# Performance work log

Measured on AMD Instinct MI355X. Metric: run time of the kernel, lower is better.

The kernel has to match this reference:

```python
import jax, jax.numpy as jnp
import numpy as np
from jax.scipy.linalg import solve_triangular, cho_solve

K_SPARSE = 5
COMMIT = 0.25
EPS = 1e-10


def batch_omp(X, D, K):
    """Batched Orthogonal Matching Pursuit.
    X: [C, M] signals (columns). D: [C, N] L2-normalized dictionary.
    Returns support [M, K] (int32) and coefficients [M, K] in selection order.
    """
    G = D.T @ D                    # [N, N] Gram matrix
    h_bar = (D.T @ X).T            # [M, N] correlations
    M, N = h_bar.shape
    h = h_bar
    mask = jnp.ones((M, N), dtype=bool)
    gamma = jnp.zeros_like(h_bar)
    L = jnp.ones((M, 1, 1), dtype=X.dtype)
    rows = jnp.arange(M)
    I = None
    for k in range(1, K + 1):  # K is small and static -> unrolled
        idx = jnp.argmax(jnp.abs(h) * mask, axis=1)          # [M]
        mask = mask.at[rows, idx].set(False)
        if k > 1:
            G_col = G[I, idx[:, None]]                        # [M, k-1]
            w = solve_triangular(L, G_col[..., None], lower=True)[..., 0]  # [M, k-1]
            corner = jnp.sqrt(jnp.clip(1.0 - jnp.sum(w * w, axis=1), 1e-12))  # [M]
            top = jnp.concatenate([L, jnp.zeros((M, k - 1, 1), X.dtype)], axis=2)
            bot = jnp.concatenate([w[:, None, :], corner[:, None, None]], axis=2)
            L = jnp.concatenate([top, bot], axis=1)           # [M, k, k]
            I = jnp.concatenate([I, idx[:, None]], axis=1)
        else:
            I = idx[:, None]
        h_sel = h_bar[rows[:, None], I]                       # [M, k]
        gamma_sel = cho_solve((L, True), h_sel[..., None])[..., 0]  # [M, k]
        gamma = gamma.at[rows[:, None], I].set(gamma_sel)
        # beta = gamma_sel @ G[I]  -> residual update over all atoms
        beta = jnp.einsum('mk,mkn->mn', gamma_sel, G[I])      # [M, N]
        h = h_bar - beta
    coeffs = gamma[rows[:, None], I]                          # [M, K]
    return I, coeffs


def setup_inputs() -> dict:
    key = jax.random.key(0)
    k1, k2 = jax.random.split(key)
    z_e = jax.random.normal(k1, (8, 64, 64, 64), dtype=jnp.float32)        # [B, C, H, W]
    dictionary = jax.random.normal(k2, (64, 512), dtype=jnp.float32)       # [C, N]
    return {"z_e": z_e, "dictionary": dictionary}


def reference(z_e, dictionary):
    B, C, H, W = z_e.shape
    # [B,C,H,W] -> [C, B*H*W] column signals
    signals = z_e.transpose(0, 2, 3, 1).reshape(-1, C).T
    # L2-normalize dictionary columns (F.normalize with dim=0)
    norms = jnp.linalg.norm(dictionary, axis=0, keepdims=True)
    Dn = dictionary / jnp.maximum(norms, EPS)
    # OMP runs under no_grad in the original
    support, coeffs = batch_omp(jax.lax.stop_gradient(signals),
                                jax.lax.stop_gradient(Dn), K_SPARSE)
    # reconstruct: sum_k coeff_k * atom_k (gradient flows through Dn)
    atoms = Dn.T[support]                                     # [M, K, C]
    recon = jnp.einsum('mkc,mk->mc', atoms, coeffs)           # [M, C]
    z_dl = recon.reshape(B, H, W, C).transpose(0, 3, 1, 2)    # [B, C, H, W]
    dl_latent_loss = jnp.mean((z_dl - jax.lax.stop_gradient(z_e)) ** 2)
    e_latent_loss = jnp.mean((jax.lax.stop_gradient(z_dl) - z_e) ** 2)
    loss = dl_latent_loss + COMMIT * e_latent_loss
    z_dl_ste = z_e + jax.lax.stop_gradient(z_dl - z_e)        # straight-through
    return (z_dl_ste, loss,
            support.reshape(B, H, W, K_SPARSE),
            coeffs.reshape(B, H, W, K_SPARSE))
```

## Files before the change

### kernel.cpp

```cpp
#include <hip/hip_runtime.h>

#define NC 64
#define NA 512
#define KS 5

#define WS_DN   0
#define WS_DNT  32768
#define WS_G    65536
#define WS_ACCF 327680

#define OUT_LOSS 2097152
#define OUT_SUP  2097153
#define OUT_COF  2260993

__global__ void norm_kernel(const float* __restrict__ D, float* __restrict__ Dn,
                            float* __restrict__ DnT) {
  int n = blockIdx.x * 64 + threadIdx.x;
  float s = 0.f;
  for (int c = 0; c < NC; ++c) {
    float v = D[c * NA + n];
    s += v * v;
  }
  float den = fmaxf(sqrtf(s), 1e-10f);
  for (int c = 0; c < NC; ++c) {
    float v = D[c * NA + n] / den;
    Dn[c * NA + n]  = v;
    DnT[n * NC + c] = v;
  }
}

__global__ void gram_kernel(const float* __restrict__ Dn,
                            float* __restrict__ G, double* __restrict__ accum) {
  __shared__ float col[NC];
  int i = blockIdx.x, t = threadIdx.x;
  if (t < NC) col[t] = Dn[t * NA + i];
  if (i == 0 && t == 0) *accum = 0.0;
  __syncthreads();
  float s = 0.f;
#pragma unroll
  for (int c = 0; c < NC; ++c) s += col[c] * Dn[c * NA + t];
  G[(size_t)i * NA + t] = s;
}

template<int KK>
__device__ __forceinline__ void omp_stepH(
    const int hl, const float* __restrict__ G,
    const float* __restrict__ parkS,
    float (&h16)[16], unsigned &msk, int (&I)[KS],
    float (&Lo)[10], float (&rd)[KS], float (&gam)[KS]) {
  float bv = -1.f; int bn = 0;
#pragma unroll
  for (int s = 0; s < 16; ++s) {
    int a = ((s >> 2) << 7) + 4 * hl + (s & 3);
    float v = ((msk >> s) & 1u) ? fabsf(h16[s]) : 0.f;
    if (v > bv) { bv = v; bn = a; }
  }
#pragma unroll
  for (int off = 1; off < 32; off <<= 1) {
    float ov = __shfl_xor(bv, off);
    int   on = __shfl_xor(bn, off);
    if (ov > bv || (ov == bv && on < bn)) { bv = ov; bn = on; }
  }
  const int idx = bn;
  if (((idx & 127) >> 2) == hl)
    msk &= ~(1u << (((idx >> 7) << 2) | (idx & 3)));
  I[KK] = idx;

  if constexpr (KK < 4) {
    const float4* pk4 = (const float4*)parkS;
#pragma unroll
    for (int i = 0; i < 4; ++i) {
      float4 hv = pk4[(i << 5) + hl];
      h16[i*4+0] = hv.x; h16[i*4+1] = hv.y; h16[i*4+2] = hv.z; h16[i*4+3] = hv.w;
    }
  }

  if constexpr (KK == 0) {
    rd[0] = 1.f;
  } else {
    float Gc[KK], w_[KK];
#pragma unroll
    for (int j = 0; j < KK; ++j) Gc[j] = G[(size_t)I[j] * NA + idx];
#pragma unroll
    for (int i = 0; i < KK; ++i) {
      float ssum = Gc[i];
#pragma unroll
      for (int j = 0; j < i; ++j) ssum -= Lo[i*(i-1)/2 + j] * w_[j];
      w_[i] = ssum * rd[i];
    }
    float ww = 0.f;
#pragma unroll
    for (int i = 0; i < KK; ++i) ww += w_[i] * w_[i];
    float corner = sqrtf(fmaxf(1.f - ww, 1e-12f));
#pragma unroll
    for (int j = 0; j < KK; ++j) Lo[KK*(KK-1)/2 + j] = w_[j];
    rd[KK] = 1.f / corner;
  }

#pragma unroll
  for (int i = 0; i <= KK; ++i) {
    float b_ = parkS[I[i]];
#pragma unroll
    for (int j = 0; j < i; ++j) b_ -= Lo[i*(i-1)/2 + j] * gam[j];
    gam[i] = b_ * rd[i];
  }
#pragma unroll
  for (int i = KK; i >= 0; --i) {
    float g_ = gam[i];
#pragma unroll
    for (int j = i + 1; j <= KK; ++j) g_ -= Lo[j*(j-1)/2 + i] * gam[j];
    gam[i] = g_ * rd[i];
  }

  if constexpr (KK < 4) {
#pragma unroll
    for (int j = 0; j <= KK; ++j) {
      const float4* g4 = (const float4*)(G + (size_t)I[j] * NA);
      const float gj = gam[j];
#pragma unroll
      for (int i = 0; i < 4; ++i) {
        float4 g = g4[(i << 5) + hl];
        h16[i*4+0] -= gj * g.x; h16[i*4+1] -= gj * g.y;
        h16[i*4+2] -= gj * g.z; h16[i*4+3] -= gj * g.w;
      }
    }
  }
}

__global__ __launch_bounds__(256, 2) void omp_kernel(
    const float* __restrict__ z, const float* __restrict__ Dn,
    const float* __restrict__ DnT, const float* __restrict__ G,
    float* __restrict__ out, double* __restrict__ accum) {
  __shared__ __align__(16) float park[8 * NA];
  __shared__ float xsz[8 * NC];
  __shared__ double wsq[8];
  const int t = threadIdx.x, lane = t & 63, wv = t >> 6;
  const int hl = lane & 31;
  const int m0 = blockIdx.x * 8;
  const int bh = m0 >> 6, b = bh >> 6, h = bh & 63, w0 = m0 & 63;
  const size_t zbase = (size_t)b * 262144 + (size_t)h * 64 + w0;

  for (int j = t; j < 8 * NC; j += 256) {
    int c = j >> 3, s = j & 7;
    xsz[s * NC + c] = z[zbase + (size_t)c * 4096 + s];
  }
  __syncthreads();
  const int sig = wv * 2 + (lane >> 5);
  const float2 xf2 = *(const float2*)&xsz[sig * NC + 2 * hl];

  {
    float acc[8][2];
#pragma unroll
    for (int s = 0; s < 8; ++s) { acc[s][0] = 0.f; acc[s][1] = 0.f; }

    const float2* Dn2 = (const float2*)Dn + (wv << 6) + lane;
    const float4* zp4 = (const float4*)(z + zbase);
#pragma unroll 8
    for (int c = 0; c < 64; ++c) {
      float2 dv = Dn2[c << 8];
      float4 xa = zp4[(c << 10)];
      float4 xb = zp4[(c << 10) + 1];
      acc[0][0] += xa.x * dv.x; acc[0][1] += xa.x * dv.y;
      acc[1][0] += xa.y * dv.x; acc[1][1] += xa.y * dv.y;
      acc[2][0] += xa.z * dv.x; acc[2][1] += xa.z * dv.y;
      acc[3][0] += xa.w * dv.x; acc[3][1] += xa.w * dv.y;
      acc[4][0] += xb.x * dv.x; acc[4][1] += xb.x * dv.y;
      acc[5][0] += xb.y * dv.x; acc[5][1] += xb.y * dv.y;
      acc[6][0] += xb.z * dv.x; acc[6][1] += xb.z * dv.y;
      acc[7][0] += xb.w * dv.x; acc[7][1] += xb.w * dv.y;
    }
    float2* park2 = (float2*)park;
#pragma unroll
    for (int s = 0; s < 8; ++s)
      park2[(s << 8) + (wv << 6) + lane] = make_float2(acc[s][0], acc[s][1]);
  }
  __syncthreads();

  const float* parkS = park + (size_t)sig * NA;
  float h16[16];
  {
    const float4* pk4 = (const float4*)parkS;
#pragma unroll
    for (int i = 0; i < 4; ++i) {
      float4 hv = pk4[(i << 5) + hl];
      h16[i*4+0] = hv.x; h16[i*4+1] = hv.y; h16[i*4+2] = hv.z; h16[i*4+3] = hv.w;
    }
  }
  unsigned msk = 0xFFFFu;
  int I[KS];
  float Lo[10], rd[KS], gam[KS];

  omp_stepH<0>(hl, G, parkS, h16, msk, I, Lo, rd, gam);
  omp_stepH<1>(hl, G, parkS, h16, msk, I, Lo, rd, gam);
  omp_stepH<2>(hl, G, parkS, h16, msk, I, Lo, rd, gam);
  omp_stepH<3>(hl, G, parkS, h16, msk, I, Lo, rd, gam);
  omp_stepH<4>(hl, G, parkS, h16, msk, I, Lo, rd, gam);

  float rrA = 0.f, rrB = 0.f;
#pragma unroll
  for (int j = 0; j < KS; ++j) {
    const float2 dvv = ((const float2*)(DnT + (size_t)I[j] * NC))[hl];
    rrA += gam[j] * dvv.x;
    rrB += gam[j] * dvv.y;
  }
  const float dA = rrA - xf2.x, dB = rrB - xf2.y;
  xsz[(2 * hl) * 8 + sig]     = xf2.x + dA;
  xsz[(2 * hl + 1) * 8 + sig] = xf2.y + dB;
  double sq = (double)dA * (double)dA + (double)dB * (double)dB;
#pragma unroll
  for (int off = 1; off < 32; off <<= 1) sq += __shfl_xor(sq, off);
  if (hl == 0) wsq[sig] = sq;

  if (hl < KS) {
    int   iv = I[0];
    float gv = gam[0];
    if (hl == 1) { iv = I[1]; gv = gam[1]; }
    if (hl == 2) { iv = I[2]; gv = gam[2]; }
    if (hl == 3) { iv = I[3]; gv = gam[3]; }
    if (hl == 4) { iv = I[4]; gv = gam[4]; }
    const int m = m0 + sig;
    out[OUT_SUP + (size_t)m * KS + hl] = (float)iv;
    out[OUT_COF + (size_t)m * KS + hl] = gv;
  }

  __syncthreads();
  for (int j = t; j < 8 * NC; j += 256) {
    int c = j >> 3, s = j & 7;
    out[zbase + (size_t)c * 4096 + s] = xsz[j];
  }
  if (t == 0) {
    double ssum = 0.0;
#pragma unroll
    for (int i = 0; i < 8; ++i) ssum += wsq[i];
    atomicAdd(accum, ssum);
  }
}

__global__ void final_kernel(const double* __restrict__ accum, float* __restrict__ out) {
  double mse = *accum / 2097152.0;
  out[OUT_LOSS] = (float)(mse + 0.25 * mse);
}

extern "C" void kernel_launch(void* const* d_in, const int* in_sizes, int n_in,
                              void* d_out, int out_size, void* d_ws, size_t ws_size,
                              hipStream_t stream) {
  const float* z_e = (const float*)d_in[0];
  const float* dic = (const float*)d_in[1];
  float* out = (float*)d_out;
  float* ws = (float*)d_ws;
  float* Dn   = ws + WS_DN;
  float* DnT  = ws + WS_DNT;
  float* G    = ws + WS_G;
  double* accu = (double*)(ws + WS_ACCF);

  hipLaunchKernelGGL(norm_kernel,  dim3(8),    dim3(64),  0, stream, dic, Dn, DnT);
  hipLaunchKernelGGL(gram_kernel,  dim3(NA),   dim3(NA),  0, stream, Dn, G, accu);
  hipLaunchKernelGGL(omp_kernel,   dim3(4096), dim3(256), 0, stream,
                     z_e, Dn, DnT, G, out, accu);
  hipLaunchKernelGGL(final_kernel, dim3(1),    dim3(1),   0, stream, accu, out);
}
```

Baseline: 152.3 us.

## Alias xsz into park LDS, fuse final loss kernel, simplify argmax

Several changes land together. The separate xsz and wsq shared buffers now alias the park buffer, which cuts LDS per block and may allow more resident blocks, at the cost of an extra barrier. The final loss kernel is folded into the OMP kernel through a last-block ticket counter, which removes one launch. The argmax becomes a two-pass max followed by a min-index reduction, and the selected h_bar value is cached in registers. Together these aim to cut launch overhead, LDS pressure and shuffle count.

```diff
diff --git a/kernel.cpp b/kernel.cpp
--- a/kernel.cpp
+++ b/kernel.cpp
@@ -30,11 +30,12 @@
 }
 
 __global__ void gram_kernel(const float* __restrict__ Dn,
-                            float* __restrict__ G, double* __restrict__ accum) {
+                            float* __restrict__ G, double* __restrict__ accum,
+                            unsigned* __restrict__ ticket) {
   __shared__ float col[NC];
   int i = blockIdx.x, t = threadIdx.x;
   if (t < NC) col[t] = Dn[t * NA + i];
-  if (i == 0 && t == 0) *accum = 0.0;
+  if (i == 0 && t == 0) { *accum = 0.0; *ticket = 0u; }
   __syncthreads();
   float s = 0.f;
 #pragma unroll
@@ -47,24 +48,32 @@
     const int hl, const float* __restrict__ G,
     const float* __restrict__ parkS,
     float (&h16)[16], unsigned &msk, int (&I)[KS],
-    float (&Lo)[10], float (&rd)[KS], float (&gam)[KS]) {
-  float bv = -1.f; int bn = 0;
-#pragma unroll
-  for (int s = 0; s < 16; ++s) {
+    float (&Lo)[10], float (&rd)[KS], float (&gam)[KS], float (&hbI)[KS]) {
+#define MVAL(s) ((((msk) >> (s)) & 1u) ? fabsf(h16[s]) : 0.f)
+  float m0 = fmaxf(MVAL(0), MVAL(1)),   m1 = fmaxf(MVAL(2), MVAL(3));
+  float m2 = fmaxf(MVAL(4), MVAL(5)),   m3 = fmaxf(MVAL(6), MVAL(7));
+  float m4 = fmaxf(MVAL(8), MVAL(9)),   m5 = fmaxf(MVAL(10), MVAL(11));
+  float m6 = fmaxf(MVAL(12), MVAL(13)), m7 = fmaxf(MVAL(14), MVAL(15));
+  float bv = fmaxf(fmaxf(fmaxf(m0, m1), fmaxf(m2, m3)),
+                   fmaxf(fmaxf(m4, m5), fmaxf(m6, m7)));
+#pragma unroll
+  for (int off = 1; off < 32; off <<= 1)
+    bv = fmaxf(bv, __shfl_xor(bv, off));
+  int cand = 0x7FFFFFFF;
+#pragma unroll
+  for (int s = 15; s >= 0; --s) {
     int a = ((s >> 2) << 7) + 4 * hl + (s & 3);
-    float v = ((msk >> s) & 1u) ? fabsf(h16[s]) : 0.f;
-    if (v > bv) { bv = v; bn = a; }
-  }
-#pragma unroll
-  for (int off = 1; off < 32; off <<= 1) {
-    float ov = __shfl_xor(bv, off);
-    int   on = __shfl_xor(bn, off);
-    if (ov > bv || (ov == bv && on < bn)) { bv = ov; bn = on; }
-  }
-  const int idx = bn;
+    if (MVAL(s) == bv) cand = a;
+  }
+#undef MVAL
+#pragma unroll
+  for (int off = 1; off < 32; off <<= 1)
+    cand = min(cand, __shfl_xor(cand, off));
+  const int idx = cand;
   if (((idx & 127) >> 2) == hl)
     msk &= ~(1u << (((idx >> 7) << 2) | (idx & 3)));
   I[KK] = idx;
+  hbI[KK] = parkS[idx];
 
   if constexpr (KK < 4) {
     const float4* pk4 = (const float4*)parkS;
@@ -99,7 +108,7 @@
 
 #pragma unroll
   for (int i = 0; i <= KK; ++i) {
-    float b_ = parkS[I[i]];
+    float b_ = hbI[i];
 #pragma unroll
     for (int j = 0; j < i; ++j) b_ -= Lo[i*(i-1)/2 + j] * gam[j];
     gam[i] = b_ * rd[i];
@@ -130,10 +139,11 @@
 __global__ __launch_bounds__(256, 2) void omp_kernel(
     const float* __restrict__ z, const float* __restrict__ Dn,
     const float* __restrict__ DnT, const float* __restrict__ G,
-    float* __restrict__ out, double* __restrict__ accum) {
+    float* __restrict__ out, double* __restrict__ accum,
+    unsigned* __restrict__ ticket) {
   __shared__ __align__(16) float park[8 * NA];
-  __shared__ float xsz[8 * NC];
-  __shared__ double wsq[8];
+  float* xsz = park;
+  double* wsq = (double*)(park + 512);
   const int t = threadIdx.x, lane = t & 63, wv = t >> 6;
   const int hl = lane & 31;
   const int m0 = blockIdx.x * 8;
@@ -148,8 +158,8 @@
   const int sig = wv * 2 + (lane >> 5);
   const float2 xf2 = *(const float2*)&xsz[sig * NC + 2 * hl];
 
+  float acc[8][2];
   {
-    float acc[8][2];
 #pragma unroll
     for (int s = 0; s < 8; ++s) { acc[s][0] = 0.f; acc[s][1] = 0.f; }
 
@@ -169,6 +179,9 @@
       acc[6][0] += xb.z * dv.x; acc[6][1] += xb.z * dv.y;
       acc[7][0] += xb.w * dv.x; acc[7][1] += xb.w * dv.y;
     }
+  }
+  __syncthreads();
+  {
     float2* park2 = (float2*)park;
 #pragma unroll
     for (int s = 0; s < 8; ++s)
@@ -188,13 +201,13 @@
   }
   unsigned msk = 0xFFFFu;
   int I[KS];
-  float Lo[10], rd[KS], gam[KS];
-
-  omp_stepH<0>(hl, G, parkS, h16, msk, I, Lo, rd, gam);
-  omp_stepH<1>(hl, G, parkS, h16, msk, I, Lo, rd, gam);
-  omp_stepH<2>(hl, G, parkS, h16, msk, I, Lo, rd, gam);
-  omp_stepH<3>(hl, G, parkS, h16, msk, I, Lo, rd, gam);
-  omp_stepH<4>(hl, G, parkS, h16, msk, I, Lo, rd, gam);
+  float Lo[10], rd[KS], gam[KS], hbI[KS];
+
+  omp_stepH<0>(hl, G, parkS, h16, msk, I, Lo, rd, gam, hbI);
+  omp_stepH<1>(hl, G, parkS, h16, msk, I, Lo, rd, gam, hbI);
+  omp_stepH<2>(hl, G, parkS, h16, msk, I, Lo, rd, gam, hbI);
+  omp_stepH<3>(hl, G, parkS, h16, msk, I, Lo, rd, gam, hbI);
+  omp_stepH<4>(hl, G, parkS, h16, msk, I, Lo, rd, gam, hbI);
 
   float rrA = 0.f, rrB = 0.f;
 #pragma unroll
@@ -204,12 +217,10 @@
     rrB += gam[j] * dvv.y;
   }
   const float dA = rrA - xf2.x, dB = rrB - xf2.y;
-  xsz[(2 * hl) * 8 + sig]     = xf2.x + dA;
-  xsz[(2 * hl + 1) * 8 + sig] = xf2.y + dB;
+  const float zoA = xf2.x + dA, zoB = xf2.y + dB;
   double sq = (double)dA * (double)dA + (double)dB * (double)dB;
 #pragma unroll
   for (int off = 1; off < 32; off <<= 1) sq += __shfl_xor(sq, off);
-  if (hl == 0) wsq[sig] = sq;
 
   if (hl < KS) {
     int   iv = I[0];
@@ -224,6 +235,10 @@
   }
 
   __syncthreads();
+  xsz[(2 * hl) * 8 + sig]     = zoA;
+  xsz[(2 * hl + 1) * 8 + sig] = zoB;
+  if (hl == 0) wsq[sig] = sq;
+  __syncthreads();
   for (int j = t; j < 8 * NC; j += 256) {
     int c = j >> 3, s = j & 7;
     out[zbase + (size_t)c * 4096 + s] = xsz[j];
@@ -233,12 +248,14 @@
 #pragma unroll
     for (int i = 0; i < 8; ++i) ssum += wsq[i];
     atomicAdd(accum, ssum);
-  }
-}
-
-__global__ void final_kernel(const double* __restrict__ accum, float* __restrict__ out) {
-  double mse = *accum / 2097152.0;
-  out[OUT_LOSS] = (float)(mse + 0.25 * mse);
+    __threadfence();
+    unsigned done = atomicAdd(ticket, 1u);
+    if (done == gridDim.x - 1) {
+      double tot = atomicAdd(accum, 0.0);
+      double mse = tot / 2097152.0;
+      out[OUT_LOSS] = (float)(mse + 0.25 * mse);
+    }
+  }
 }
 
 extern "C" void kernel_launch(void* const* d_in, const int* in_sizes, int n_in,
@@ -252,10 +269,10 @@
   float* DnT  = ws + WS_DNT;
   float* G    = ws + WS_G;
   double* accu = (double*)(ws + WS_ACCF);
+  unsigned* ticket = (unsigned*)(ws + WS_ACCF + 2);
 
   hipLaunchKernelGGL(norm_kernel,  dim3(8),    dim3(64),  0, stream, dic, Dn, DnT);
-  hipLaunchKernelGGL(gram_kernel,  dim3(NA),   dim3(NA),  0, stream, Dn, G, accu);
+  hipLaunchKernelGGL(gram_kernel,  dim3(NA),   dim3(NA),  0, stream, Dn, G, accu, ticket);
   hipLaunchKernelGGL(omp_kernel,   dim3(4096), dim3(256), 0, stream,
-                     z_e, Dn, DnT, G, out, accu);
-  hipLaunchKernelGGL(final_kernel, dim3(1),    dim3(1),   0, stream, accu, out);
-}
+                     z_e, Dn, DnT, G, out, accu, ticket);
+}
```

Measured after the change: 256.6 us. 68.5% more time.
